# Kernel tuning notes

Hardware: AMD Instinct MI355X
Metric: run time of the kernel (lower is better)

## Reference

```python
import jax, jax.numpy as jnp
import numpy as np

N_NODES = 50000
N_EDGES = 800000
D_FEAT = 64
D_EMB = 64
N_GRAPHS = 512
D_TARGET = 10


def setup_inputs() -> dict:
    key = jax.random.key(0)
    ks = jax.random.split(key, 32)
    x = jax.random.normal(ks[0], (N_NODES, D_FEAT), dtype=jnp.float32)
    edge_index = jax.random.randint(ks[1], (2, N_EDGES), 0, N_NODES, dtype=jnp.int64)
    batch = jnp.sort(jax.random.randint(ks[2], (N_NODES,), 0, N_GRAPHS, dtype=jnp.int64))

    def lin(k, fan_in, fan_out):
        return jax.random.normal(k, (fan_in, fan_out), dtype=jnp.float32) / np.sqrt(fan_in)

    inp = {"x": x, "edge_index": edge_index, "batch": batch}
    # 3 SAGEConv layers: lin_l (neighbors, with bias) + lin_r (root, no bias)
    for i in range(3):
        din = D_FEAT if i == 0 else D_EMB
        inp[f"Wl{i}"] = lin(ks[3 + 3 * i], din, D_EMB)
        inp[f"bl{i}"] = jnp.zeros((D_EMB,), dtype=jnp.float32)
        inp[f"Wr{i}"] = lin(ks[4 + 3 * i], din, D_EMB)
    inp["Wm"] = lin(ks[20], D_EMB, D_EMB)
    inp["bm"] = jnp.zeros((D_EMB,), dtype=jnp.float32)
    inp["W1"] = lin(ks[21], 3 * D_EMB, D_EMB)
    inp["b1"] = jnp.zeros((D_EMB,), dtype=jnp.float32)
    inp["W2"] = lin(ks[22], D_EMB, D_TARGET)
    inp["b2"] = jnp.zeros((D_TARGET,), dtype=jnp.float32)
    return inp


def sage_conv(x, src, dst, Wl, bl, Wr):
    # mean-aggregate neighbor features (messages flow src -> dst)
    agg = jax.ops.segment_sum(x[src], dst, num_segments=N_NODES)
    deg = jax.ops.segment_sum(jnp.ones((src.shape[0],), x.dtype), dst, num_segments=N_NODES)
    mean = agg / jnp.maximum(deg, 1.0)[:, None]
    return mean @ Wl + bl + x @ Wr


def reference(x, edge_index, batch, Wl0, bl0, Wr0, Wl1, bl1, Wr1, Wl2, bl2, Wr2,
              Wm, bm, W1, b1, W2, b2):
    src, dst = edge_index[0], edge_index[1]
    convs = [(Wl0, bl0, Wr0), (Wl1, bl1, Wr1), (Wl2, bl2, Wr2)]
    h = x
    h_all = []
    for Wl, bl, Wr in convs:
        h = sage_conv(h, src, dst, Wl, bl, Wr)
        h = jax.nn.relu(h @ Wm + bm)
        h_all.append(h)
    h = jnp.concatenate(h_all, axis=1)  # [N, 3*D_EMB]
    # global mean pool over graphs
    gsum = jax.ops.segment_sum(h, batch, num_segments=N_GRAPHS)
    gcnt = jax.ops.segment_sum(jnp.ones((h.shape[0],), h.dtype), batch, num_segments=N_GRAPHS)
    g = gsum / jnp.maximum(gcnt, 1.0)[:, None]
    g = jax.nn.relu(g @ W1 + b1)
    return g @ W2 + b2
```

## Files before the change

### kernel.cpp

```cpp
#include <hip/hip_runtime.h>

#define N_NODES 50000
#define N_EDGES 800000
#define D 64
#define N_GRAPHS 512
#define D_TARGET 10
#define NB_SCAN ((N_NODES + 255) / 256)
#define TPAD 72

typedef __attribute__((ext_vector_type(8))) short short8;
typedef __attribute__((ext_vector_type(4))) float f32x4;
typedef unsigned short ushort_t;
#define MFMA16(a, b, c) __builtin_amdgcn_mfma_f32_16x16x32_bf16(a, b, c, 0, 0, 0)

__device__ inline unsigned short bf16rne(float f) {
    unsigned u = __builtin_bit_cast(unsigned, f);
    u += 0x7FFFu + ((u >> 16) & 1u);
    return (unsigned short)(u >> 16);
}
__device__ inline float bf2f(unsigned short h) {
    unsigned u = ((unsigned)h) << 16;
    return __builtin_bit_cast(float, u);
}
__device__ inline void acc8(float* a, uint4 v) {
    a[0] += __builtin_bit_cast(float, v.x << 16);
    a[1] += __builtin_bit_cast(float, v.x & 0xFFFF0000u);
    a[2] += __builtin_bit_cast(float, v.y << 16);
    a[3] += __builtin_bit_cast(float, v.y & 0xFFFF0000u);
    a[4] += __builtin_bit_cast(float, v.z << 16);
    a[5] += __builtin_bit_cast(float, v.z & 0xFFFF0000u);
    a[6] += __builtin_bit_cast(float, v.w << 16);
    a[7] += __builtin_bit_cast(float, v.w & 0xFFFF0000u);
}

__global__ void count_kernel(const int* __restrict__ dst, int* __restrict__ degi) {
    int i = blockIdx.x * blockDim.x + threadIdx.x;
    if (i < N_EDGES) atomicAdd(&degi[dst[i]], 1);
}

__global__ void scan_partials(const int* __restrict__ degi, int* __restrict__ partial) {
    __shared__ int s[256];
    int t = threadIdx.x;
    int i = blockIdx.x * 256 + t;
    s[t] = (i < N_NODES) ? degi[i] : 0;
    __syncthreads();
    for (int off = 128; off > 0; off >>= 1) {
        if (t < off) s[t] += s[t + off];
        __syncthreads();
    }
    if (t == 0) partial[blockIdx.x] = s[0];
}

__global__ void scan_offsets(int* __restrict__ partial) {
    if (threadIdx.x == 0) {
        int run = 0;
        for (int i = 0; i < NB_SCAN; ++i) { int p = partial[i]; partial[i] = run; run += p; }
    }
}

__global__ void scan_final(const int* __restrict__ degi, const int* __restrict__ partial,
                           int* __restrict__ rowptr, int* __restrict__ next) {
    __shared__ int s[256];
    int t = threadIdx.x;
    int i = blockIdx.x * 256 + t;
    int v = (i < N_NODES) ? degi[i] : 0;
    s[t] = v;
    __syncthreads();
    for (int off = 1; off < 256; off <<= 1) {
        int add = (t >= off) ? s[t - off] : 0;
        __syncthreads();
        s[t] += add;
        __syncthreads();
    }
    if (i < N_NODES) {
        int excl = partial[blockIdx.x] + s[t] - v;
        rowptr[i] = excl;
        next[i]   = excl;
    }
    if (i == 0) rowptr[N_NODES] = N_EDGES;
}

__global__ void fill_kernel(const int* __restrict__ src, const int* __restrict__ dst,
                            int* __restrict__ next, ushort_t* __restrict__ col) {
    int e = blockIdx.x * blockDim.x + threadIdx.x;
    if (e < N_EDGES) {
        int pos = atomicAdd(&next[dst[e]], 1);
        col[pos] = (ushort_t)src[e];
    }
}

__global__ void gstart_kernel(const int* __restrict__ batch, int* __restrict__ gstart) {
    int i = blockIdx.x * 256 + threadIdx.x;
    if (i >= N_NODES) return;
    int b = batch[i];
    int prev = (i == 0) ? -1 : batch[i - 1];
    for (int g = prev + 1; g <= b; ++g) gstart[g] = i;
    if (i == N_NODES - 1)
        for (int g = b + 1; g <= N_GRAPHS; ++g) gstart[g] = N_NODES;
}

__global__ void wprep_kernel(const float* __restrict__ w0, const float* __restrict__ w1,
                             const float* __restrict__ w2, const float* __restrict__ w3,
                             const float* __restrict__ w4, const float* __restrict__ w5,
                             const float* __restrict__ w6, short* __restrict__ out) {
    int tid = blockIdx.x * 256 + threadIdx.x;
    int m = tid >> 12, t = tid & 4095;
    const float* W = (m == 0) ? w0 : (m == 1) ? w1 : (m == 2) ? w2 : (m == 3) ? w3
                   : (m == 4) ? w4 : (m == 5) ? w5 : w6;
    int j = t & 7, lane = (t >> 3) & 63, nt = (t >> 9) & 3, kt = t >> 11;
    int k = kt * 32 + ((lane >> 4) << 3) + j;
    int o = nt * 16 + (lane & 15);
    float v = W[k * 64 + o];
    unsigned short hi = bf16rne(v);
    unsigned short lo = bf16rne(v - bf2f(hi));
    out[m * 8192 + t]        = (short)hi;
    out[m * 8192 + 4096 + t] = (short)lo;
}

__global__ void xsplit_kernel(const float* __restrict__ x, ushort_t* __restrict__ xh) {
    int i = blockIdx.x * 256 + threadIdx.x;
    if (i < N_NODES * D) xh[i] = bf16rne(x[i]);
}

__global__ __launch_bounds__(512) void gather_kernel(
    const ushort_t* __restrict__ hplane, const int* __restrict__ rowptr,
    const ushort_t* __restrict__ col,
    ushort_t* __restrict__ mh, ushort_t* __restrict__ ml) {
    int gw   = (blockIdx.x * 512 + threadIdx.x) >> 6;
    int lane = threadIdx.x & 63;
    int f = lane & 7;
    int g = lane >> 3;
    if (gw >= N_NODES) return;
    int beg = rowptr[gw], end = rowptr[gw + 1];
    const uint4* h16 = (const uint4*)hplane;

    float a[8] = {0.f, 0.f, 0.f, 0.f, 0.f, 0.f, 0.f, 0.f};
    float b[8] = {0.f, 0.f, 0.f, 0.f, 0.f, 0.f, 0.f, 0.f};
    int p = beg + g;
    for (; p + 8 < end; p += 16) {
        int s0 = col[p], s1 = col[p + 8];
        uint4 v0 = h16[s0 * 8 + f];
        uint4 v1 = h16[s1 * 8 + f];
        acc8(a, v0);
        acc8(b, v1);
    }
    if (p < end) {
        uint4 v = h16[col[p] * 8 + f];
        acc8(a, v);
    }
#pragma unroll
    for (int j = 0; j < 8; ++j) {
        float v = a[j] + b[j];
        v += __shfl_xor(v, 8);
        v += __shfl_xor(v, 16);
        v += __shfl_xor(v, 32);
        a[j] = v;
    }
    if (g == 0) {
        float inv = 1.0f / fmaxf((float)(end - beg), 1.0f);
        unsigned hws[4], lws[4];
#pragma unroll
        for (int i = 0; i < 4; ++i) {
            float v0 = a[2 * i] * inv, v1 = a[2 * i + 1] * inv;
            unsigned short h0 = bf16rne(v0), h1 = bf16rne(v1);
            hws[i] = (unsigned)h0 | ((unsigned)h1 << 16);
            lws[i] = (unsigned)bf16rne(v0 - bf2f(h0)) |
                     ((unsigned)bf16rne(v1 - bf2f(h1)) << 16);
        }
        uint4 hv = {hws[0], hws[1], hws[2], hws[3]};
        uint4 lv = {lws[0], lws[1], lws[2], lws[3]};
        ((uint4*)mh)[gw * 8 + f] = hv;
        ((uint4*)ml)[gw * 8 + f] = lv;
    }
}

template <int XMODE>
__global__ __launch_bounds__(64) void mm_kernel(
    const float* __restrict__ xf, const ushort_t* __restrict__ xhp,
    const ushort_t* __restrict__ mh, const ushort_t* __restrict__ ml,
    const short* __restrict__ wl, const short* __restrict__ wr, const short* __restrict__ wm,
    const float* __restrict__ blv, const float* __restrict__ bmv,
    ushort_t* __restrict__ hhout) {
    __shared__ short smh[16 * TPAD];
    __shared__ short sml[16 * TPAD];
    __shared__ short sxh[16 * TPAD];
    __shared__ short sxl[16 * TPAD];
    __shared__ short sth[16 * TPAD];
    __shared__ short stl[16 * TPAD];

    int lane = threadIdx.x;
    int f = lane & 15;
    int g = lane >> 4;
    int base = blockIdx.x * 16;

    {
        const uint4* mh16 = (const uint4*)mh;
        const uint4* ml16 = (const uint4*)ml;
#pragma unroll
        for (int i = 0; i < 2; ++i) {
            int c = i * 64 + lane;
            int r = c >> 3, cc = c & 7;
            *(uint4*)&smh[r * TPAD + cc * 8] = mh16[(base + r) * 8 + cc];
            *(uint4*)&sml[r * TPAD + cc * 8] = ml16[(base + r) * 8 + cc];
        }
    }
    if (XMODE == 1) {
        const uint4* xh16 = (const uint4*)xhp;
#pragma unroll
        for (int i = 0; i < 2; ++i) {
            int c = i * 64 + lane;
            int r = c >> 3, cc = c & 7;
            *(uint4*)&sxh[r * TPAD + cc * 8] = xh16[(base + r) * 8 + cc];
        }
    } else {
        const float4* x4 = (const float4*)xf;
#pragma unroll
        for (int i = 0; i < 4; ++i) {
            int idx = i * 64 + lane;
            int r = idx >> 4, c = idx & 15;
            float4 xv = x4[(size_t)(base + r) * 16 + c];
            unsigned short h0 = bf16rne(xv.x), h1 = bf16rne(xv.y),
                           h2 = bf16rne(xv.z), h3 = bf16rne(xv.w);
            uint2 hw, lw;
            hw.x = (unsigned)h0 | ((unsigned)h1 << 16);
            hw.y = (unsigned)h2 | ((unsigned)h3 << 16);
            lw.x = (unsigned)bf16rne(xv.x - bf2f(h0)) | ((unsigned)bf16rne(xv.y - bf2f(h1)) << 16);
            lw.y = (unsigned)bf16rne(xv.z - bf2f(h2)) | ((unsigned)bf16rne(xv.w - bf2f(h3)) << 16);
            *(uint2*)&sxh[r * TPAD + c * 4] = hw;
            *(uint2*)&sxl[r * TPAD + c * 4] = lw;
        }
    }

    short8 amh[2], aml[2], axh[2], axl[2];
#pragma unroll
    for (int kt = 0; kt < 2; ++kt) {
        int idx = f * TPAD + kt * 32 + g * 8;
        amh[kt] = *(const short8*)&smh[idx];
        aml[kt] = *(const short8*)&sml[idx];
        axh[kt] = *(const short8*)&sxh[idx];
        if (XMODE == 0) axl[kt] = *(const short8*)&sxl[idx];
    }
    const short* wlh = wl;
    const short* wll = wl + 4096;
    const short* wrh = wr;
    const short* wrl = wr + 4096;

#pragma unroll
    for (int nt = 0; nt < 4; ++nt) {
        f32x4 acc = {0.f, 0.f, 0.f, 0.f};
#pragma unroll
        for (int kt = 0; kt < 2; ++kt) {
            int fi = ((kt * 4 + nt) * 64 + lane) * 8;
            short8 blh = *(const short8*)&wlh[fi];
            short8 bll = *(const short8*)&wll[fi];
            short8 brh = *(const short8*)&wrh[fi];
            short8 brl = *(const short8*)&wrl[fi];
            acc = MFMA16(amh[kt], blh, acc);
            acc = MFMA16(aml[kt], blh, acc);
            acc = MFMA16(amh[kt], bll, acc);
            acc = MFMA16(axh[kt], brh, acc);
            if (XMODE == 0) acc = MFMA16(axl[kt], brh, acc);
            acc = MFMA16(axh[kt], brl, acc);
        }
        float bias = blv[nt * 16 + f];
#pragma unroll
        for (int r = 0; r < 4; ++r) {
            float tv = acc[r] + bias;
            unsigned short hi = bf16rne(tv);
            unsigned short lo = bf16rne(tv - bf2f(hi));
            int row = g * 4 + r;
            sth[row * TPAD + nt * 16 + f] = (short)hi;
            stl[row * TPAD + nt * 16 + f] = (short)lo;
        }
    }

    short8 ath[2], atl[2];
#pragma unroll
    for (int kt = 0; kt < 2; ++kt) {
        int idx = f * TPAD + kt * 32 + g * 8;
        ath[kt] = *(const short8*)&sth[idx];
        atl[kt] = *(const short8*)&stl[idx];
    }
    const short* wmh = wm;
    const short* wml = wm + 4096;
#pragma unroll
    for (int nt = 0; nt < 4; ++nt) {
        f32x4 acc = {0.f, 0.f, 0.f, 0.f};
#pragma unroll
        for (int kt = 0; kt < 2; ++kt) {
            int fi = ((kt * 4 + nt) * 64 + lane) * 8;
            short8 bh  = *(const short8*)&wmh[fi];
            short8 bl2 = *(const short8*)&wml[fi];
            acc = MFMA16(ath[kt], bh, acc);
            acc = MFMA16(atl[kt], bh, acc);
            acc = MFMA16(ath[kt], bl2, acc);
        }
        float bias = bmv[nt * 16 + f];
#pragma unroll
        for (int r = 0; r < 4; ++r) {
            float hv = acc[r] + bias;
            hv = hv > 0.f ? hv : 0.f;
            int row  = g * 4 + r;
            int node = base + row;
            hhout[node * D + nt * 16 + f] = bf16rne(hv);
        }
    }
}

__global__ __launch_bounds__(256) void poolmlp_kernel(
    const ushort_t* __restrict__ h0, const ushort_t* __restrict__ h1,
    const ushort_t* __restrict__ h2, const int* __restrict__ gstart,
    const float* __restrict__ W1, const float* __restrict__ b1,
    const float* __restrict__ W2, const float* __restrict__ b2,
    float* __restrict__ out) {
    __shared__ float spart[4][3][64];
    __shared__ float sg[3 * 64];
    __shared__ float tt[64];
    int gr = blockIdx.x;
    int w = threadIdx.x >> 6, lane = threadIdx.x & 63;
    int beg = gstart[gr], end = gstart[gr + 1];
    float s0 = 0.f, s1 = 0.f, s2 = 0.f;
    for (int n = beg + w; n < end; n += 4) {
        s0 += bf2f(h0[n * 64 + lane]);
        s1 += bf2f(h1[n * 64 + lane]);
        s2 += bf2f(h2[n * 64 + lane]);
    }
    spart[w][0][lane] = s0; spart[w][1][lane] = s1; spart[w][2][lane] = s2;
    __syncthreads();
    if (w == 0) {
        float inv = 1.0f / fmaxf((float)(end - beg), 1.0f);
#pragma unroll
        for (int l = 0; l < 3; ++l)
            sg[l * 64 + lane] = (spart[0][l][lane] + spart[1][l][lane] +
                                 spart[2][l][lane] + spart[3][l][lane]) * inv;
    }
    __syncthreads();
    if (w == 0) {
        float acc = b1[lane];
#pragma unroll 8
        for (int k = 0; k < 3 * 64; ++k) acc += sg[k] * W1[k * 64 + lane];
        tt[lane] = fmaxf(acc, 0.f);
    }
    __syncthreads();
    if (w == 0 && lane < D_TARGET) {
        float acc = b2[lane];
#pragma unroll
        for (int k = 0; k < 64; ++k) acc += tt[k] * W2[k * D_TARGET + lane];
        out[gr * D_TARGET + lane] = acc;
    }
}

extern "C" void kernel_launch(void* const* d_in, const int* in_sizes, int n_in,
                              void* d_out, int out_size, void* d_ws, size_t ws_size,
                              hipStream_t stream) {
    const float* x     = (const float*)d_in[0];
    const int*   ei    = (const int*)d_in[1];
    const int*   src   = ei;
    const int*   dst   = ei + N_EDGES;
    const int*   batch = (const int*)d_in[2];

    const float* Wl[3] = {(const float*)d_in[3], (const float*)d_in[6], (const float*)d_in[9]};
    const float* bl[3] = {(const float*)d_in[4], (const float*)d_in[7], (const float*)d_in[10]};
    const float* Wr[3] = {(const float*)d_in[5], (const float*)d_in[8], (const float*)d_in[11]};
    const float* Wm = (const float*)d_in[12];
    const float* bm = (const float*)d_in[13];
    const float* W1 = (const float*)d_in[14];
    const float* b1 = (const float*)d_in[15];
    const float* W2 = (const float*)d_in[16];
    const float* b2 = (const float*)d_in[17];

    int*      degi    = (int*)d_ws;
    int*      partial = degi + 50000;
    int*      rowptr  = partial + 256;
    int*      next    = rowptr + 50008;
    int*      gstart  = next + 50000;
    short*    wfrag   = (short*)(gstart + 520);
    ushort_t* col     = (ushort_t*)(wfrag + 7 * 8192);
    ushort_t* xh      = col + 800000;
    ushort_t* mh      = xh + (size_t)N_NODES * D;
    ushort_t* ml      = mh + (size_t)N_NODES * D;
    ushort_t* hh0     = ml + (size_t)N_NODES * D;
    ushort_t* hh1     = hh0 + (size_t)N_NODES * D;
    ushort_t* hh2     = hh1 + (size_t)N_NODES * D;

    hipMemsetAsync(degi, 0, 50000 * sizeof(int), stream);

    count_kernel<<<(N_EDGES + 255) / 256, 256, 0, stream>>>(dst, degi);
    scan_partials<<<NB_SCAN, 256, 0, stream>>>(degi, partial);
    scan_offsets<<<1, 64, 0, stream>>>(partial);
    scan_final<<<NB_SCAN, 256, 0, stream>>>(degi, partial, rowptr, next);
    fill_kernel<<<(N_EDGES + 255) / 256, 256, 0, stream>>>(src, dst, next, col);
    gstart_kernel<<<NB_SCAN, 256, 0, stream>>>(batch, gstart);
    wprep_kernel<<<7 * 4096 / 256, 256, 0, stream>>>(
        Wl[0], Wr[0], Wl[1], Wr[1], Wl[2], Wr[2], Wm, wfrag);
    xsplit_kernel<<<(N_NODES * D + 255) / 256, 256, 0, stream>>>(x, xh);

    ushort_t* hplanes[4] = {xh, hh0, hh1, hh2};
    for (int l = 0; l < 3; ++l) {
        gather_kernel<<<(N_NODES * 64 + 511) / 512, 512, 0, stream>>>(
            hplanes[l], rowptr, col, mh, ml);
        if (l == 0)
            mm_kernel<0><<<N_NODES / 16, 64, 0, stream>>>(
                x, nullptr, mh, ml,
                wfrag + 0 * 8192, wfrag + 1 * 8192, wfrag + 6 * 8192,
                bl[0], bm, hh0);
        else
            mm_kernel<1><<<N_NODES / 16, 64, 0, stream>>>(
                nullptr, hplanes[l], mh, ml,
                wfrag + (2 * l) * 8192, wfrag + (2 * l + 1) * 8192, wfrag + 6 * 8192,
                bl[l], bm, hplanes[l + 1]);
    }

    poolmlp_kernel<<<N_GRAPHS, 256, 0, stream>>>(hh0, hh1, hh2, gstart, W1, b1, W2, b2,
                                                 (float*)d_out);
}
```

Measured before the change: 222.0 us.

## Merge preprocessing kernels, fold offset scan into scan_final, bin fill atomics by destination

```diff
diff --git a/kernel.cpp b/kernel.cpp
--- a/kernel.cpp
+++ b/kernel.cpp
@@ -7,6 +7,12 @@
 #define D_TARGET 10
 #define NB_SCAN ((N_NODES + 255) / 256)
 #define TPAD 72
+#define NBIN 8
+#define NODES_PER_BIN (N_NODES / NBIN)
+#define EDGE_BLOCKS (N_EDGES / 256)
+#define FILL_BLOCKS (NBIN * EDGE_BLOCKS)
+#define XSPLIT_BLOCKS EDGE_BLOCKS
+#define WPREP_BLOCKS 112
 
 typedef __attribute__((ext_vector_type(8))) short short8;
 typedef __attribute__((ext_vector_type(4))) float f32x4;
@@ -33,9 +39,21 @@
     a[7] += __builtin_bit_cast(float, v.w & 0xFFFF0000u);
 }
 
-__global__ void count_kernel(const int* __restrict__ dst, int* __restrict__ degi) {
-    int i = blockIdx.x * blockDim.x + threadIdx.x;
-    if (i < N_EDGES) atomicAdd(&degi[dst[i]], 1);
+__global__ void k1_kernel(const int* __restrict__ dst, const int* __restrict__ batch,
+                          int* __restrict__ degi, int* __restrict__ gstart) {
+    int b = blockIdx.x;
+    if (b < EDGE_BLOCKS) {
+        int e = b * 256 + threadIdx.x;
+        atomicAdd(&degi[dst[e]], 1);
+    } else {
+        int i = (b - EDGE_BLOCKS) * 256 + threadIdx.x;
+        if (i >= N_NODES) return;
+        int bb = batch[i];
+        int prev = (i == 0) ? -1 : batch[i - 1];
+        for (int g = prev + 1; g <= bb; ++g) gstart[g] = i;
+        if (i == N_NODES - 1)
+            for (int g = bb + 1; g <= N_GRAPHS; ++g) gstart[g] = N_NODES;
+    }
 }
 
 __global__ void scan_partials(const int* __restrict__ degi, int* __restrict__ partial) {
@@ -51,18 +69,19 @@
     if (t == 0) partial[blockIdx.x] = s[0];
 }
 
-__global__ void scan_offsets(int* __restrict__ partial) {
-    if (threadIdx.x == 0) {
-        int run = 0;
-        for (int i = 0; i < NB_SCAN; ++i) { int p = partial[i]; partial[i] = run; run += p; }
-    }
-}
-
 __global__ void scan_final(const int* __restrict__ degi, const int* __restrict__ partial,
                            int* __restrict__ rowptr, int* __restrict__ next) {
     __shared__ int s[256];
+    __shared__ int sp[256];
     int t = threadIdx.x;
     int i = blockIdx.x * 256 + t;
+    sp[t] = (t < blockIdx.x) ? partial[t] : 0;
+    __syncthreads();
+    for (int off = 128; off > 0; off >>= 1) {
+        if (t < off) sp[t] += sp[t + off];
+        __syncthreads();
+    }
+    int prefix = sp[0];
     int v = (i < N_NODES) ? degi[i] : 0;
     s[t] = v;
     __syncthreads();
@@ -73,53 +92,50 @@
         __syncthreads();
     }
     if (i < N_NODES) {
-        int excl = partial[blockIdx.x] + s[t] - v;
+        int excl = prefix + s[t] - v;
         rowptr[i] = excl;
         next[i]   = excl;
     }
     if (i == 0) rowptr[N_NODES] = N_EDGES;
 }
 
-__global__ void fill_kernel(const int* __restrict__ src, const int* __restrict__ dst,
-                            int* __restrict__ next, ushort_t* __restrict__ col) {
-    int e = blockIdx.x * blockDim.x + threadIdx.x;
-    if (e < N_EDGES) {
-        int pos = atomicAdd(&next[dst[e]], 1);
-        col[pos] = (ushort_t)src[e];
-    }
-}
-
-__global__ void gstart_kernel(const int* __restrict__ batch, int* __restrict__ gstart) {
-    int i = blockIdx.x * 256 + threadIdx.x;
-    if (i >= N_NODES) return;
-    int b = batch[i];
-    int prev = (i == 0) ? -1 : batch[i - 1];
-    for (int g = prev + 1; g <= b; ++g) gstart[g] = i;
-    if (i == N_NODES - 1)
-        for (int g = b + 1; g <= N_GRAPHS; ++g) gstart[g] = N_NODES;
-}
-
-__global__ void wprep_kernel(const float* __restrict__ w0, const float* __restrict__ w1,
-                             const float* __restrict__ w2, const float* __restrict__ w3,
-                             const float* __restrict__ w4, const float* __restrict__ w5,
-                             const float* __restrict__ w6, short* __restrict__ out) {
-    int tid = blockIdx.x * 256 + threadIdx.x;
-    int m = tid >> 12, t = tid & 4095;
-    const float* W = (m == 0) ? w0 : (m == 1) ? w1 : (m == 2) ? w2 : (m == 3) ? w3
-                   : (m == 4) ? w4 : (m == 5) ? w5 : w6;
-    int j = t & 7, lane = (t >> 3) & 63, nt = (t >> 9) & 3, kt = t >> 11;
-    int k = kt * 32 + ((lane >> 4) << 3) + j;
-    int o = nt * 16 + (lane & 15);
-    float v = W[k * 64 + o];
-    unsigned short hi = bf16rne(v);
-    unsigned short lo = bf16rne(v - bf2f(hi));
-    out[m * 8192 + t]        = (short)hi;
-    out[m * 8192 + 4096 + t] = (short)lo;
-}
-
-__global__ void xsplit_kernel(const float* __restrict__ x, ushort_t* __restrict__ xh) {
-    int i = blockIdx.x * 256 + threadIdx.x;
-    if (i < N_NODES * D) xh[i] = bf16rne(x[i]);
+__global__ void k4_kernel(const int* __restrict__ src, const int* __restrict__ dst,
+                          int* __restrict__ next, ushort_t* __restrict__ col,
+                          const float* __restrict__ x, ushort_t* __restrict__ xh,
+                          const float* __restrict__ w0, const float* __restrict__ w1,
+                          const float* __restrict__ w2, const float* __restrict__ w3,
+                          const float* __restrict__ w4, const float* __restrict__ w5,
+                          const float* __restrict__ w6, short* __restrict__ wfrag) {
+    int b = blockIdx.x;
+    if (b < FILL_BLOCKS) {
+        int bin = b / EDGE_BLOCKS;
+        int e = (b % EDGE_BLOCKS) * 256 + threadIdx.x;
+        int d = dst[e];
+        int lo = bin * NODES_PER_BIN;
+        if (d >= lo && d < lo + NODES_PER_BIN) {
+            int pos = atomicAdd(&next[d], 1);
+            col[pos] = (ushort_t)src[e];
+        }
+    } else if (b < FILL_BLOCKS + XSPLIT_BLOCKS) {
+        int idx = (b - FILL_BLOCKS) * 256 + threadIdx.x;
+        float4 v = ((const float4*)x)[idx];
+        ushort4 o;
+        o.x = bf16rne(v.x); o.y = bf16rne(v.y); o.z = bf16rne(v.z); o.w = bf16rne(v.w);
+        ((ushort4*)xh)[idx] = o;
+    } else {
+        int tid = (b - FILL_BLOCKS - XSPLIT_BLOCKS) * 256 + threadIdx.x;
+        int m = tid >> 12, t = tid & 4095;
+        const float* W = (m == 0) ? w0 : (m == 1) ? w1 : (m == 2) ? w2 : (m == 3) ? w3
+                       : (m == 4) ? w4 : (m == 5) ? w5 : w6;
+        int j = t & 7, lane = (t >> 3) & 63, nt = (t >> 9) & 3, kt = t >> 11;
+        int k = kt * 32 + ((lane >> 4) << 3) + j;
+        int o = nt * 16 + (lane & 15);
+        float v = W[k * 64 + o];
+        unsigned short hi = bf16rne(v);
+        unsigned short lo = bf16rne(v - bf2f(hi));
+        wfrag[m * 8192 + t]        = (short)hi;
+        wfrag[m * 8192 + 4096 + t] = (short)lo;
+    }
 }
 
 __global__ __launch_bounds__(512) void gather_kernel(
@@ -385,15 +401,12 @@
 
     hipMemsetAsync(degi, 0, 50000 * sizeof(int), stream);
 
-    count_kernel<<<(N_EDGES + 255) / 256, 256, 0, stream>>>(dst, degi);
+    k1_kernel<<<EDGE_BLOCKS + NB_SCAN, 256, 0, stream>>>(dst, batch, degi, gstart);
     scan_partials<<<NB_SCAN, 256, 0, stream>>>(degi, partial);
-    scan_offsets<<<1, 64, 0, stream>>>(partial);
     scan_final<<<NB_SCAN, 256, 0, stream>>>(degi, partial, rowptr, next);
-    fill_kernel<<<(N_EDGES + 255) / 256, 256, 0, stream>>>(src, dst, next, col);
-    gstart_kernel<<<NB_SCAN, 256, 0, stream>>>(batch, gstart);
-    wprep_kernel<<<7 * 4096 / 256, 256, 0, stream>>>(
+    k4_kernel<<<FILL_BLOCKS + XSPLIT_BLOCKS + WPREP_BLOCKS, 256, 0, stream>>>(
+        src, dst, next, col, x, xh,
         Wl[0], Wr[0], Wl[1], Wr[1], Wl[2], Wr[2], Wm, wfrag);
-    xsplit_kernel<<<(N_NODES * D + 255) / 256, 256, 0, stream>>>(x, xh);
 
     ushort_t* hplanes[4] = {xh, hh0, hh1, hh2};
     for (int l = 0; l < 3; ++l) {
```

Result: faster. 214.4 us (-3.4%).
